# Kernel optimization log

Measured on AMD Instinct MI355X. Metric: run time of the kernel, lower is better.

The kernel has to match this reference:

```python
import jax, jax.numpy as jnp
import numpy as np

EPS = 1e-5        # module's self.eps
CLAMP = 1e-8      # numerical floor for norms
BS, H, W, C = 64, 64, 64, 128


def linner(x, y):
    """Lorentz inner product -x0*y0 + <x_s, y_s>, keepdims on last axis."""
    xy = jnp.sum(x * y, axis=-1, keepdims=True)
    return xy - 2.0 * (x[..., :1] * y[..., :1])


def setup_inputs() -> dict:
    key = jax.random.key(0)
    k1 = jax.random.fold_in(key, 1)
    # random points on the unit hyperboloid (k=1): x0 = sqrt(1 + ||x_s||^2)
    xs = 0.5 * jax.random.normal(k1, (BS, H, W, C - 1), jnp.float32)
    x0 = jnp.sqrt(1.0 + jnp.sum(xs * xs, axis=-1, keepdims=True))
    x = jnp.concatenate([x0, xs], axis=-1)
    beta = jnp.zeros((C,), jnp.float32).at[0].set(1.0)  # manifold origin
    gamma = jnp.ones((1,), jnp.float32)
    return {"x": x, "beta": beta, "gamma": gamma}


def _lorentz_batchnorm(x, beta, gamma):
    bs, h, w, c = x.shape
    x = x.reshape(bs, h * w, c)                                   # [bs,N,c]
    e0 = jnp.zeros((c,), x.dtype).at[0].set(1.0)

    # centroid: Euclidean mean re-projected onto the hyperboloid
    m = jnp.mean(x, axis=1, keepdims=True)                        # [bs,1,c]
    mean = m / jnp.sqrt(jnp.clip(-linner(m, m), CLAMP))           # [bs,1,c]

    # logmap_mean(x): d(mean,x) * (x - alpha*mean) / ||.||_L, alpha = -<mean,x>_L
    alpha = jnp.clip(-linner(mean, x), 1.0 + 1e-7)                # [bs,N,1]
    u = x - alpha * mean
    un = jnp.sqrt(jnp.clip(linner(u, u), CLAMP))
    x_T = jnp.arccosh(alpha) * u / un                             # tangent @ mean

    # parallel transport mean -> origin: u - u0/(1+mean0) * (mean + e0)
    x_T = x_T - (x_T[..., :1] / (1.0 + mean[..., :1])) * (mean + e0)

    # Frechet variance (mean Euclidean norm of tangent vectors)
    var = jnp.mean(jnp.linalg.norm(x_T, axis=-1), axis=1, keepdims=True)  # [bs,1]
    x_T = x_T * (gamma / (var[..., None] + EPS))

    # parallel transport origin -> beta: u + <beta,u>_L/(1+beta0) * (beta + e0)
    x_T = x_T + (linner(beta, x_T) / (1.0 + beta[0])) * (beta + e0)

    # expmap at beta
    nu = jnp.sqrt(jnp.clip(linner(x_T, x_T), CLAMP))
    out = jnp.cosh(nu) * beta + jnp.sinh(nu) * x_T / nu
    return out.reshape(bs, h, w, c)


def reference(x, beta, gamma):
    return _lorentz_batchnorm(x, beta, gamma)
```

## Files before the change

kernel.cpp:

```cpp
#include <hip/hip_runtime.h>
#include <math.h>

#define BS    64
#define NROWS 4096
#define CCH   128
#define NC4   32
#define BPB   32
#define RPB   (NROWS/BPB)

typedef float vf4 __attribute__((ext_vector_type(4)));

__device__ __forceinline__ float dot4(float4 a, float4 b) {
    return a.x*b.x + a.y*b.y + a.z*b.z + a.w*b.w;
}

__global__ __launch_bounds__(256) void k_mean_sum(const float4* __restrict__ x,
                                                  float* __restrict__ msum) {
    int b   = blockIdx.x / BPB;
    int blk = blockIdx.x % BPB;
    int t   = threadIdx.x;
    int c4  = t & 31;
    int grp = t >> 5;
    int row0 = blk * RPB;
    const float4* xb = x + (size_t)b * NROWS * NC4;

    float4 acc = make_float4(0.f, 0.f, 0.f, 0.f);
    for (int r = row0 + grp; r < row0 + RPB; r += 8) {
        float4 v = xb[(size_t)r * NC4 + c4];
        acc.x += v.x; acc.y += v.y; acc.z += v.z; acc.w += v.w;
    }
    __shared__ float4 lds[256];
    lds[t] = acc;
    __syncthreads();
    if (t < 32) {
        float4 s = lds[t];
        #pragma unroll
        for (int k = 1; k < 8; ++k) {
            float4 v = lds[t + 32 * k];
            s.x += v.x; s.y += v.y; s.z += v.z; s.w += v.w;
        }
        atomicAdd(&msum[b * CCH + 4 * t + 0], s.x);
        atomicAdd(&msum[b * CCH + 4 * t + 1], s.y);
        atomicAdd(&msum[b * CCH + 4 * t + 2], s.z);
        atomicAdd(&msum[b * CCH + 4 * t + 3], s.w);
    }
}

__global__ __launch_bounds__(256) void k_rows(const float4* __restrict__ x,
                                              const float* __restrict__ msum,
                                              const float* __restrict__ beta,
                                              float* __restrict__ mean,
                                              float* __restrict__ varsum,
                                              float4* __restrict__ rowp) {
    int blk = blockIdx.x;
    int b   = blk >> 4;
    int sub = blk & 15;
    int t   = threadIdx.x;

    __shared__ float  sm[128];
    __shared__ float4 mvs[32];
    __shared__ float4 bvs[32];
    __shared__ float2 red2[256];
    __shared__ float  redh[256];

    float m = 0.f, bc = 0.f;
    if (t < 128) {
        m  = msum[b * CCH + t] * (1.0f / (float)NROWS);
        bc = beta[t];
        sm[t] = m;
    }
    red2[t] = make_float2(m * m, bc * m);
    __syncthreads();
    #pragma unroll
    for (int s = 128; s > 0; s >>= 1) {
        if (t < s) { red2[t].x += red2[t + s].x; red2[t].y += red2[t + s].y; }
        __syncthreads();
    }
    float smm = red2[0].x, sbm = red2[0].y;
    float m0  = sm[0];
    float val = fmaf(2.f * m0, m0, -smm);
    float inv = __builtin_amdgcn_rsqf(fmaxf(val, 1e-8f));
    float mean0   = m0 * inv;
    float inv1pm0 = __builtin_amdgcn_rcpf(1.0f + mean0);
    float b0  = beta[0];
    float lbm = (sbm - 2.f * b0 * m0) * inv;
    if (t < 128) {
        float mc = sm[t] * inv;
        ((float*)mvs)[t] = mc;
        ((float*)bvs)[t] = bc;
        if (sub == 0) mean[b * CCH + t] = mc;
    }
    __syncthreads();

    int lane = t & 63, wave = t >> 6;
    int q  = lane >> 2;
    int ql = lane & 3;
    int srcl = lane & ~3;
    float nsum = 0.f;

    #pragma unroll
    for (int o = 0; o < 4; ++o) {
        int row = sub * 256 + o * 64 + wave * 16 + q;
        const float4* xr = x + ((size_t)b * NROWS + row) * NC4;

        float4 xv = xr[ql];
        float4 mv = mvs[ql];
        float4 bv = bvs[ql];
        float x00 = xv.x;
        float d = dot4(xv, mv);
        float e = dot4(xv, bv);
        #pragma unroll
        for (int c = 1; c < 8; ++c) {
            int c4 = 4 * c + ql;
            xv = xr[c4];
            mv = mvs[c4];
            bv = bvs[c4];
            d = fmaf(xv.x, mv.x, fmaf(xv.y, mv.y, fmaf(xv.z, mv.z, fmaf(xv.w, mv.w, d))));
            e = fmaf(xv.x, bv.x, fmaf(xv.y, bv.y, fmaf(xv.z, bv.z, fmaf(xv.w, bv.w, e))));
        }
        d += __shfl_xor(d, 1);  e += __shfl_xor(e, 1);
        d += __shfl_xor(d, 2);  e += __shfl_xor(e, 2);
        float x0 = __shfl(x00, srcl);

        float alpha = fmaxf(fmaf(2.f * mean0, x0, -d), 1.0f + 1e-7f);
        float a2m1  = fmaxf(fmaf(alpha, alpha, -1.f), 1e-8f);
        float sq    = sqrtf(a2m1);
        float h     = __logf(alpha + sq);
        float fac   = h * __builtin_amdgcn_rcpf(sq);
        float u0    = fmaf(-alpha, mean0, x0);
        float tc    = fac * u0 * inv1pm0;
        float s_m   = fmaf(fac, alpha, tc);
        float lbx   = fmaf(-2.f * b0, x0, e);
        float pb    = fmaf(fac, lbx, fmaf(-s_m, lbm, tc * b0));
        if (ql == 0) rowp[(size_t)b * NROWS + row] = make_float4(fac, alpha, tc, pb);
        nsum += 0.25f * h;
    }

    redh[t] = nsum;
    __syncthreads();
    #pragma unroll
    for (int s = 128; s > 0; s >>= 1) {
        if (t < s) redh[t] += redh[t + s];
        __syncthreads();
    }
    if (t == 0) atomicAdd(&varsum[b], redh[0]);
}

__global__ __launch_bounds__(256) void k_out(const float4* __restrict__ x,
                                             const float* __restrict__ mean,
                                             const float* __restrict__ varsum,
                                             const float* __restrict__ beta,
                                             const float* __restrict__ gamma,
                                             const float4* __restrict__ rowp,
                                             float4* __restrict__ out) {
    int b   = blockIdx.x / BPB;
    int blk = blockIdx.x % BPB;
    int t   = threadIdx.x;
    int c4  = t & 31;
    int grp = t >> 5;

    const float* meanb = mean + b * CCH;
    float4 mv = ((const float4*)meanb)[c4];
    float4 bv = ((const float4*)beta)[c4];
    float  b0 = beta[0];
    float  invb  = __builtin_amdgcn_rcpf(1.0f + b0);
    float  scale = gamma[0] * __builtin_amdgcn_rcpf(
                        varsum[b] * (1.0f / (float)NROWS) + 1e-5f);

    const float4* xb = x + (size_t)b * NROWS * NC4;
    float4*       ob = out + (size_t)b * NROWS * NC4;
    int row0 = blk * RPB;

    for (int r = row0 + grp; r < row0 + RPB; r += 8) {
        float4 xv = xb[(size_t)r * NC4 + c4];
        float4 rp = rowp[(size_t)b * NROWS + r];
        float fac = rp.x, alpha = rp.y, tcv = rp.z, pb = rp.w;

        float F   = scale * fac;
        float TCv = scale * tcv;
        float SM  = fmaf(F, alpha, TCv);
        float sq  = sqrtf(fmaxf(fmaf(alpha, alpha, -1.f), 1e-8f));
        float nu  = fmaxf(scale * (fac * sq), 1e-4f);
        float PT  = scale * pb * invb;

        float ee = __expf(nu);
        float ei = __builtin_amdgcn_rcpf(ee);
        float ch = 0.5f * (ee + ei);
        float so = 0.5f * (ee - ei) * __builtin_amdgcn_rcpf(nu);

        float A = so * F;
        float B = -so * SM;
        float C = fmaf(so, PT, ch);
        float D = so * (PT - TCv);

        vf4 ov;
        ov.x = fmaf(A, xv.x, fmaf(B, mv.x, C * bv.x));
        ov.y = fmaf(A, xv.y, fmaf(B, mv.y, C * bv.y));
        ov.z = fmaf(A, xv.z, fmaf(B, mv.z, C * bv.z));
        ov.w = fmaf(A, xv.w, fmaf(B, mv.w, C * bv.w));
        if (c4 == 0) ov.x += D;
        __builtin_nontemporal_store(ov, (vf4*)&ob[(size_t)r * NC4 + c4]);
    }
}

extern "C" void kernel_launch(void* const* d_in, const int* in_sizes, int n_in,
                              void* d_out, int out_size, void* d_ws, size_t ws_size,
                              hipStream_t stream) {
    const float* x     = (const float*)d_in[0];
    const float* beta  = (const float*)d_in[1];
    const float* gamma = (const float*)d_in[2];
    float*       out   = (float*)d_out;

    float* ws     = (float*)d_ws;
    float* msum   = ws;
    float* varsum = ws + 8192;
    float* mean   = ws + 8256;
    float4* rowp  = (float4*)((char*)d_ws + 65792);

    hipMemsetAsync(ws, 0, (8192 + 64) * sizeof(float), stream);

    k_mean_sum<<<dim3(BS * BPB), dim3(256), 0, stream>>>((const float4*)x, msum);
    k_rows<<<dim3(1024), dim3(256), 0, stream>>>(
        (const float4*)x, msum, beta, mean, varsum, rowp);
    k_out<<<dim3(BS * BPB), dim3(256), 0, stream>>>(
        (const float4*)x, mean, varsum, beta, gamma, rowp, (float4*)out);
}
```

Before: 282.9 us.

## Fuse three batchnorm kernels into one cooperative kernel with grid syncs

```diff
diff --git a/kernel.cpp b/kernel.cpp
--- a/kernel.cpp
+++ b/kernel.cpp
@@ -1,18 +1,203 @@
 #include <hip/hip_runtime.h>
+#include <hip/hip_cooperative_groups.h>
 #include <math.h>
 
-#define BS    64
+namespace cg = cooperative_groups;
+
+#define BSZ   64
 #define NROWS 4096
 #define CCH   128
 #define NC4   32
-#define BPB   32
-#define RPB   (NROWS/BPB)
 
 typedef float vf4 __attribute__((ext_vector_type(4)));
 
 __device__ __forceinline__ float dot4(float4 a, float4 b) {
     return a.x*b.x + a.y*b.y + a.z*b.z + a.w*b.w;
 }
+
+#define RPB 256
+
+__global__ __launch_bounds__(256, 4) void k_fused(
+        const float4* __restrict__ x,
+        const float*  __restrict__ beta,
+        const float*  __restrict__ gamma,
+        float*        __restrict__ msum2,
+        float*        __restrict__ varpart,
+        float4*       __restrict__ out) {
+    cg::grid_group grid = cg::this_grid();
+    const int blk  = blockIdx.x;
+    const int b    = blk >> 4;
+    const int sub  = blk & 15;
+    const int t    = threadIdx.x;
+    const int row0 = sub * RPB;
+
+    __shared__ float4 lds4[256];
+    __shared__ float4 mvs[32];
+    __shared__ float4 bvs[32];
+    __shared__ float  sm[128];
+    __shared__ float2 red2[256];
+    __shared__ float  redh[256];
+    __shared__ float4 rowp[RPB];
+
+    const float4* xb = x + ((size_t)b * NROWS + row0) * NC4;
+
+    {
+        const int c4  = t & 31;
+        const int grp = t >> 5;
+        float4 acc = make_float4(0.f, 0.f, 0.f, 0.f);
+        for (int r = grp; r < RPB; r += 8) {
+            float4 v = xb[(size_t)r * NC4 + c4];
+            acc.x += v.x; acc.y += v.y; acc.z += v.z; acc.w += v.w;
+        }
+        lds4[t] = acc;
+        __syncthreads();
+        if (t < 32) {
+            float4 s = lds4[t];
+            #pragma unroll
+            for (int k = 1; k < 8; ++k) {
+                float4 v = lds4[t + 32*k];
+                s.x += v.x; s.y += v.y; s.z += v.z; s.w += v.w;
+            }
+            ((float4*)(msum2 + (size_t)blk * CCH))[t] = make_float4(s.x, s.y, s.z, s.w);
+        }
+    }
+    grid.sync();
+
+    float m = 0.f, bc = 0.f;
+    if (t < CCH) {
+        float s = 0.f;
+        #pragma unroll
+        for (int k = 0; k < 16; ++k)
+            s += msum2[(size_t)((b << 4) + k) * CCH + t];
+        m  = s * (1.0f / (float)NROWS);
+        bc = beta[t];
+        sm[t] = m;
+    }
+    red2[t] = make_float2(m * m, bc * m);
+    __syncthreads();
+    #pragma unroll
+    for (int s = 128; s > 0; s >>= 1) {
+        if (t < s) { red2[t].x += red2[t + s].x; red2[t].y += red2[t + s].y; }
+        __syncthreads();
+    }
+    const float smm = red2[0].x, sbm = red2[0].y;
+    const float m0  = sm[0];
+    const float val = fmaf(2.f * m0, m0, -smm);
+    const float inv = __builtin_amdgcn_rsqf(fmaxf(val, 1e-8f));
+    const float mean0   = m0 * inv;
+    const float inv1pm0 = __builtin_amdgcn_rcpf(1.0f + mean0);
+    const float b0  = beta[0];
+    const float lbm = (sbm - 2.f * b0 * m0) * inv;
+    if (t < CCH) {
+        ((float*)mvs)[t] = sm[t] * inv;
+        ((float*)bvs)[t] = bc;
+    }
+    __syncthreads();
+
+    {
+        const int lane = t & 63, wave = t >> 6;
+        const int q    = lane >> 2;
+        const int ql   = lane & 3;
+        const int srcl = lane & ~3;
+        float nsum = 0.f;
+
+        #pragma unroll
+        for (int o = 0; o < 4; ++o) {
+            const int lrow = o * 64 + wave * 16 + q;
+            const float4* xr = xb + (size_t)lrow * NC4;
+
+            float4 xv = xr[ql];
+            float4 mv = mvs[ql];
+            float4 bv = bvs[ql];
+            float x00 = xv.x;
+            float d = dot4(xv, mv);
+            float e = dot4(xv, bv);
+            #pragma unroll
+            for (int c = 1; c < 8; ++c) {
+                int c4i = 4 * c + ql;
+                xv = xr[c4i];
+                mv = mvs[c4i];
+                bv = bvs[c4i];
+                d = fmaf(xv.x, mv.x, fmaf(xv.y, mv.y, fmaf(xv.z, mv.z, fmaf(xv.w, mv.w, d))));
+                e = fmaf(xv.x, bv.x, fmaf(xv.y, bv.y, fmaf(xv.z, bv.z, fmaf(xv.w, bv.w, e))));
+            }
+            d += __shfl_xor(d, 1);  e += __shfl_xor(e, 1);
+            d += __shfl_xor(d, 2);  e += __shfl_xor(e, 2);
+            float x0 = __shfl(x00, srcl);
+
+            float alpha = fmaxf(fmaf(2.f * mean0, x0, -d), 1.0f + 1e-7f);
+            float a2m1  = fmaxf(fmaf(alpha, alpha, -1.f), 1e-8f);
+            float sq    = sqrtf(a2m1);
+            float h     = __logf(alpha + sq);
+            float fac   = h * __builtin_amdgcn_rcpf(sq);
+            float u0    = fmaf(-alpha, mean0, x0);
+            float tc    = fac * u0 * inv1pm0;
+            float s_m   = fmaf(fac, alpha, tc);
+            float lbx   = fmaf(-2.f * b0, x0, e);
+            float pb    = fmaf(fac, lbx, fmaf(-s_m, lbm, tc * b0));
+            if (ql == 0) rowp[lrow] = make_float4(fac, alpha, tc, pb);
+            nsum += 0.25f * h;
+        }
+        redh[t] = nsum;
+    }
+    __syncthreads();
+    #pragma unroll
+    for (int s = 128; s > 0; s >>= 1) {
+        if (t < s) redh[t] += redh[t + s];
+        __syncthreads();
+    }
+    if (t == 0) varpart[blk] = redh[0];
+
+    grid.sync();
+
+    {
+        float vsum = 0.f;
+        #pragma unroll
+        for (int k = 0; k < 16; ++k) vsum += varpart[(b << 4) + k];
+        const float scale = gamma[0] * __builtin_amdgcn_rcpf(
+                                vsum * (1.0f / (float)NROWS) + 1e-5f);
+        const float invb  = __builtin_amdgcn_rcpf(1.0f + b0);
+        const int c4  = t & 31;
+        const int grp = t >> 5;
+        const float4 mv = mvs[c4];
+        const float4 bv = bvs[c4];
+        float4* ob = out + ((size_t)b * NROWS + row0) * NC4;
+
+        for (int r = grp; r < RPB; r += 8) {
+            float4 xv = xb[(size_t)r * NC4 + c4];
+            float4 rp = rowp[r];
+            float fac = rp.x, alpha = rp.y, tcv = rp.z, pb = rp.w;
+
+            float F   = scale * fac;
+            float TCv = scale * tcv;
+            float SM  = fmaf(F, alpha, TCv);
+            float sq  = sqrtf(fmaxf(fmaf(alpha, alpha, -1.f), 1e-8f));
+            float nu  = fmaxf(scale * (fac * sq), 1e-4f);
+            float PT  = scale * pb * invb;
+
+            float ee = __expf(nu);
+            float ei = __builtin_amdgcn_rcpf(ee);
+            float ch = 0.5f * (ee + ei);
+            float so = 0.5f * (ee - ei) * __builtin_amdgcn_rcpf(nu);
+
+            float A = so * F;
+            float B = -so * SM;
+            float C = fmaf(so, PT, ch);
+            float D = so * (PT - TCv);
+
+            vf4 ov;
+            ov.x = fmaf(A, xv.x, fmaf(B, mv.x, C * bv.x));
+            ov.y = fmaf(A, xv.y, fmaf(B, mv.y, C * bv.y));
+            ov.z = fmaf(A, xv.z, fmaf(B, mv.z, C * bv.z));
+            ov.w = fmaf(A, xv.w, fmaf(B, mv.w, C * bv.w));
+            if (c4 == 0) ov.x += D;
+            __builtin_nontemporal_store(ov, (vf4*)&ob[(size_t)r * NC4 + c4]);
+        }
+    }
+}
+
+#define BPB  32
+#define RPBF (NROWS/BPB)
 
 __global__ __launch_bounds__(256) void k_mean_sum(const float4* __restrict__ x,
                                                   float* __restrict__ msum) {
@@ -21,11 +206,11 @@
     int t   = threadIdx.x;
     int c4  = t & 31;
     int grp = t >> 5;
-    int row0 = blk * RPB;
+    int row0 = blk * RPBF;
     const float4* xb = x + (size_t)b * NROWS * NC4;
 
     float4 acc = make_float4(0.f, 0.f, 0.f, 0.f);
-    for (int r = row0 + grp; r < row0 + RPB; r += 8) {
+    for (int r = row0 + grp; r < row0 + RPBF; r += 8) {
         float4 v = xb[(size_t)r * NC4 + c4];
         acc.x += v.x; acc.y += v.y; acc.z += v.z; acc.w += v.w;
     }
@@ -51,7 +236,7 @@
                                               const float* __restrict__ beta,
                                               float* __restrict__ mean,
                                               float* __restrict__ varsum,
-                                              float4* __restrict__ rowp) {
+                                              float4* __restrict__ rowpg) {
     int blk = blockIdx.x;
     int b   = blk >> 4;
     int sub = blk & 15;
@@ -132,7 +317,7 @@
         float s_m   = fmaf(fac, alpha, tc);
         float lbx   = fmaf(-2.f * b0, x0, e);
         float pb    = fmaf(fac, lbx, fmaf(-s_m, lbm, tc * b0));
-        if (ql == 0) rowp[(size_t)b * NROWS + row] = make_float4(fac, alpha, tc, pb);
+        if (ql == 0) rowpg[(size_t)b * NROWS + row] = make_float4(fac, alpha, tc, pb);
         nsum += 0.25f * h;
     }
 
@@ -151,7 +336,7 @@
                                              const float* __restrict__ varsum,
                                              const float* __restrict__ beta,
                                              const float* __restrict__ gamma,
-                                             const float4* __restrict__ rowp,
+                                             const float4* __restrict__ rowpg,
                                              float4* __restrict__ out) {
     int b   = blockIdx.x / BPB;
     int blk = blockIdx.x % BPB;
@@ -169,11 +354,11 @@
 
     const float4* xb = x + (size_t)b * NROWS * NC4;
     float4*       ob = out + (size_t)b * NROWS * NC4;
-    int row0 = blk * RPB;
-
-    for (int r = row0 + grp; r < row0 + RPB; r += 8) {
+    int row0 = blk * RPBF;
+
+    for (int r = row0 + grp; r < row0 + RPBF; r += 8) {
         float4 xv = xb[(size_t)r * NC4 + c4];
-        float4 rp = rowp[(size_t)b * NROWS + r];
+        float4 rp = rowpg[(size_t)b * NROWS + r];
         float fac = rp.x, alpha = rp.y, tcv = rp.z, pb = rp.w;
 
         float F   = scale * fac;
@@ -206,22 +391,31 @@
 extern "C" void kernel_launch(void* const* d_in, const int* in_sizes, int n_in,
                               void* d_out, int out_size, void* d_ws, size_t ws_size,
                               hipStream_t stream) {
-    const float* x     = (const float*)d_in[0];
-    const float* beta  = (const float*)d_in[1];
-    const float* gamma = (const float*)d_in[2];
-    float*       out   = (float*)d_out;
-
-    float* ws     = (float*)d_ws;
-    float* msum   = ws;
-    float* varsum = ws + 8192;
-    float* mean   = ws + 8256;
-    float4* rowp  = (float4*)((char*)d_ws + 65792);
-
-    hipMemsetAsync(ws, 0, (8192 + 64) * sizeof(float), stream);
-
-    k_mean_sum<<<dim3(BS * BPB), dim3(256), 0, stream>>>((const float4*)x, msum);
-    k_rows<<<dim3(1024), dim3(256), 0, stream>>>(
-        (const float4*)x, msum, beta, mean, varsum, rowp);
-    k_out<<<dim3(BS * BPB), dim3(256), 0, stream>>>(
-        (const float4*)x, mean, varsum, beta, gamma, rowp, (float4*)out);
-}
+    const float4* x     = (const float4*)d_in[0];
+    const float*  beta  = (const float*)d_in[1];
+    const float*  gamma = (const float*)d_in[2];
+    float4*       out   = (float4*)d_out;
+
+    float* msum2   = (float*)d_ws;
+    float* varpart = msum2 + 1024 * CCH;
+
+    void* args[6] = { (void*)&x, (void*)&beta, (void*)&gamma,
+                      (void*)&msum2, (void*)&varpart, (void*)&out };
+    hipError_t err = hipLaunchCooperativeKernel((const void*)k_fused,
+                                                dim3(1024), dim3(256),
+                                                args, 0, stream);
+    if (err != hipSuccess) {
+        float* ws     = (float*)d_ws;
+        float* msum   = ws;
+        float* varsum = ws + 8192;
+        float* mean   = ws + 8256;
+        float4* rowpg = (float4*)((char*)d_ws + 65792);
+
+        hipMemsetAsync(ws, 0, (8192 + 64) * sizeof(float), stream);
+        k_mean_sum<<<dim3(BSZ * BPB), dim3(256), 0, stream>>>(x, msum);
+        k_rows<<<dim3(1024), dim3(256), 0, stream>>>(
+            x, msum, beta, mean, varsum, rowpg);
+        k_out<<<dim3(BSZ * BPB), dim3(256), 0, stream>>>(
+            x, mean, varsum, beta, gamma, rowpg, out);
+    }
+}
```

New measurement: 483.9 us. 71.1% more time.
